# Kernel tuning notes

Measured on AMD Instinct MI355X. Metric: run time of the kernel, lower is better.

## Reference

```python
import jax, jax.numpy as jnp
import numpy as np

B, T, C, H = 4, 2048, 1024, 16
D = C // H  # head_dim = 64


def setup_inputs() -> dict:
    key = jax.random.key(0)
    k1, k2, k3 = jax.random.split(key, 3)
    x = jax.random.normal(k1, (B, T, C), dtype=jnp.float32)
    w_attn = jax.random.normal(k2, (C, 3 * C), dtype=jnp.float32) * (1.0 / np.sqrt(C))
    b_attn = jnp.zeros((3 * C,), dtype=jnp.float32)
    w_proj = jax.random.normal(k3, (C, C), dtype=jnp.float32) * (1.0 / np.sqrt(C))
    b_proj = jnp.zeros((C,), dtype=jnp.float32)
    return {"x": x, "w_attn": w_attn, "b_attn": b_attn, "w_proj": w_proj, "b_proj": b_proj}


def reference(x, w_attn, b_attn, w_proj, b_proj):
    Bx, Tx, Cx = x.shape
    qkv = x @ w_attn + b_attn                      # (B, T, 3C)
    q, k, v = jnp.split(qkv, 3, axis=2)
    # (B, T, C) -> (B, H, T, D)
    q = q.reshape(Bx, Tx, H, D).transpose(0, 2, 1, 3)
    k = k.reshape(Bx, Tx, H, D).transpose(0, 2, 1, 3)
    v = v.reshape(Bx, Tx, H, D).transpose(0, 2, 1, 3)
    scores = jnp.einsum('bhqd,bhkd->bhqk', q, k) / jnp.sqrt(jnp.float32(D))
    causal = jnp.tril(jnp.ones((Tx, Tx), dtype=bool))
    scores = jnp.where(causal[None, None], scores, jnp.float32(-jnp.inf))
    probs = jax.nn.softmax(scores, axis=-1)
    out = jnp.einsum('bhqk,bhkd->bhqd', probs, v)  # (B, H, T, D)
    out = out.transpose(0, 2, 1, 3).reshape(Bx, Tx, Cx)
    return out @ w_proj + b_proj
```

## Files before the change

### kernel.cpp

```cpp
#include <hip/hip_runtime.h>

#define AS1 __attribute__((address_space(1)))
#define AS3 __attribute__((address_space(3)))

using bf16x8  = __attribute__((ext_vector_type(8))) __bf16;
using floatx4 = __attribute__((ext_vector_type(4))) float;

#define SCQ 0.18033688f

__device__ inline ushort f2b(float f) {
    __bf16 h = (__bf16)f;
    return __builtin_bit_cast(ushort, h);
}

__global__ void k_prep(const float* __restrict__ x, ushort* __restrict__ xb,
                       const float* __restrict__ wa, ushort* __restrict__ waT,
                       const float* __restrict__ wp, ushort* __restrict__ wpT)
{
    __shared__ float tile[32][33];
    int blk = blockIdx.x;
    if (blk < 8192) {
        int i = (blk * 256 + threadIdx.x) * 4;
        float4 v = *(const float4*)(x + i);
        ushort4 o;
        o.x = f2b(v.x); o.y = f2b(v.y); o.z = f2b(v.z); o.w = f2b(v.w);
        *(ushort4*)(xb + i) = o;
        return;
    }
    const float* in; ushort* out; int R, Ncol, bx, by; float scale; int scale_cols;
    if (blk < 11264) {
        int idx = blk - 8192;
        in = wa; out = waT; R = 1024; Ncol = 3072;
        bx = idx % 96; by = idx / 96; scale = SCQ; scale_cols = 1024;
    } else {
        int idx = blk - 11264;
        in = wp; out = wpT; R = 1024; Ncol = 1024;
        bx = idx % 32; by = idx / 32; scale = 1.0f; scale_cols = 0;
    }
    int tx = threadIdx.x & 31, ty = threadIdx.x >> 5;
    int c0 = bx * 32, r0 = by * 32;
    for (int i = 0; i < 32; i += 8)
        tile[ty + i][tx] = in[(size_t)(r0 + ty + i) * Ncol + c0 + tx];
    __syncthreads();
    for (int i = 0; i < 32; i += 8) {
        int n = c0 + ty + i;
        float v = tile[tx][ty + i];
        if (n < scale_cols) v *= scale;
        out[(size_t)n * R + r0 + tx] = f2b(v);
    }
}

__global__ __launch_bounds__(256, 2) void k_gemm_bt(
    const ushort* __restrict__ A, const ushort* __restrict__ Bt,
    const float* __restrict__ bias, float* __restrict__ outv,
    int M, int N, int K)
{
    __shared__ __align__(16) ushort As[128 * 64];
    __shared__ __align__(16) ushort Bs[128 * 64];
    int tid = threadIdx.x;
    int m0 = blockIdx.y * 128, n0 = blockIdx.x * 128;
    int lane = tid & 63;
    int wm = (tid >> 7) * 64;
    int wn = ((tid >> 6) & 1) * 64;
    int lr = lane & 15, quad = lane >> 4;

    floatx4 acc[4][4] = {};
    const ushort* ags[4]; const ushort* bgs[4]; int sdst[4];
    #pragma unroll
    for (int it = 0; it < 4; ++it) {
        int slot = tid + 256 * it;
        int row = slot >> 3, ch = slot & 7;
        ags[it] = A  + (size_t)(m0 + row) * K + ch * 8;
        bgs[it] = Bt + (size_t)(n0 + row) * K + ch * 8;
        sdst[it] = slot * 8;
    }

    for (int kt = 0; kt < K; kt += 64) {
        #pragma unroll
        for (int it = 0; it < 4; ++it) {
            __builtin_amdgcn_global_load_lds((const AS1 unsigned int*)(ags[it] + kt),
                                             (AS3 unsigned int*)&As[sdst[it]], 16, 0, 0);
            __builtin_amdgcn_global_load_lds((const AS1 unsigned int*)(bgs[it] + kt),
                                             (AS3 unsigned int*)&Bs[sdst[it]], 16, 0, 0);
        }
        asm volatile("s_waitcnt vmcnt(0)" ::: "memory");
        __syncthreads();
        bf16x8 af[4][2], bf[4][2];
        #pragma unroll
        for (int i = 0; i < 4; ++i) {
            af[i][0] = *(const bf16x8*)&As[(wm + 16 * i + lr) * 64 + quad * 8];
            af[i][1] = *(const bf16x8*)&As[(wm + 16 * i + lr) * 64 + 32 + quad * 8];
        }
        #pragma unroll
        for (int j = 0; j < 4; ++j) {
            bf[j][0] = *(const bf16x8*)&Bs[(wn + 16 * j + lr) * 64 + quad * 8];
            bf[j][1] = *(const bf16x8*)&Bs[(wn + 16 * j + lr) * 64 + 32 + quad * 8];
        }
        #pragma unroll
        for (int i = 0; i < 4; ++i)
            #pragma unroll
            for (int j = 0; j < 4; ++j) {
                acc[i][j] = __builtin_amdgcn_mfma_f32_16x16x32_bf16(af[i][0], bf[j][0], acc[i][j], 0, 0, 0);
                acc[i][j] = __builtin_amdgcn_mfma_f32_16x16x32_bf16(af[i][1], bf[j][1], acc[i][j], 0, 0, 0);
            }
        __syncthreads();
    }

    #pragma unroll
    for (int j = 0; j < 4; ++j) {
        int col = n0 + wn + 16 * j + lr;
        float bv = bias[col];
        #pragma unroll
        for (int i = 0; i < 4; ++i) {
            int row = m0 + wm + 16 * i + quad * 4;
            #pragma unroll
            for (int r = 0; r < 4; ++r)
                outv[(size_t)(row + r) * N + col] = acc[i][j][r] + bv;
        }
    }
}

__global__ __launch_bounds__(256, 2) void k_gemm_qkv(
    const ushort* __restrict__ A, const ushort* __restrict__ Bt,
    const float* __restrict__ bias, ushort* __restrict__ qkv, ushort* __restrict__ vt)
{
    constexpr int K = 1024;
    __shared__ __align__(16) ushort As[128 * 64];
    __shared__ __align__(16) ushort Bs[128 * 64];
    int tid = threadIdx.x;
    int m0 = blockIdx.y * 128, n0 = blockIdx.x * 128;
    int lane = tid & 63;
    int wm = (tid >> 7) * 64;
    int wn = ((tid >> 6) & 1) * 64;
    int lr = lane & 15, quad = lane >> 4;

    floatx4 acc[4][4] = {};
    const ushort* ags[4]; const ushort* bgs[4]; int sdst[4];
    #pragma unroll
    for (int it = 0; it < 4; ++it) {
        int slot = tid + 256 * it;
        int row = slot >> 3, ch = slot & 7;
        ags[it] = A  + (size_t)(m0 + row) * K + ch * 8;
        bgs[it] = Bt + (size_t)(n0 + row) * K + ch * 8;
        sdst[it] = slot * 8;
    }

    for (int kt = 0; kt < K; kt += 64) {
        #pragma unroll
        for (int it = 0; it < 4; ++it) {
            __builtin_amdgcn_global_load_lds((const AS1 unsigned int*)(ags[it] + kt),
                                             (AS3 unsigned int*)&As[sdst[it]], 16, 0, 0);
            __builtin_amdgcn_global_load_lds((const AS1 unsigned int*)(bgs[it] + kt),
                                             (AS3 unsigned int*)&Bs[sdst[it]], 16, 0, 0);
        }
        asm volatile("s_waitcnt vmcnt(0)" ::: "memory");
        __syncthreads();
        bf16x8 af[4][2], bf[4][2];
        #pragma unroll
        for (int i = 0; i < 4; ++i) {
            af[i][0] = *(const bf16x8*)&As[(wm + 16 * i + lr) * 64 + quad * 8];
            af[i][1] = *(const bf16x8*)&As[(wm + 16 * i + lr) * 64 + 32 + quad * 8];
        }
        #pragma unroll
        for (int j = 0; j < 4; ++j) {
            bf[j][0] = *(const bf16x8*)&Bs[(wn + 16 * j + lr) * 64 + quad * 8];
            bf[j][1] = *(const bf16x8*)&Bs[(wn + 16 * j + lr) * 64 + 32 + quad * 8];
        }
        #pragma unroll
        for (int i = 0; i < 4; ++i)
            #pragma unroll
            for (int j = 0; j < 4; ++j) {
                acc[i][j] = __builtin_amdgcn_mfma_f32_16x16x32_bf16(af[i][0], bf[j][0], acc[i][j], 0, 0, 0);
                acc[i][j] = __builtin_amdgcn_mfma_f32_16x16x32_bf16(af[i][1], bf[j][1], acc[i][j], 0, 0, 0);
            }
        __syncthreads();
    }

    int bb = m0 >> 11;
    #pragma unroll
    for (int j = 0; j < 4; ++j) {
        int col = n0 + wn + 16 * j + lr;
        float bv = bias[col];
        if (col < 1024) bv *= SCQ;
        if (col < 2048) {
            #pragma unroll
            for (int i = 0; i < 4; ++i) {
                int row = m0 + wm + 16 * i + quad * 4;
                #pragma unroll
                for (int r = 0; r < 4; ++r)
                    qkv[(size_t)(row + r) * 2048 + col] = f2b(acc[i][j][r] + bv);
            }
        } else {
            int h = (col - 2048) >> 6, d = (col - 2048) & 63;
            ushort* vbase = vt + ((size_t)(bb * 16 + h) * 64 + d) * 2048;
            #pragma unroll
            for (int i = 0; i < 4; ++i) {
                int t0 = (m0 + wm + 16 * i + quad * 4) & 2047;
                ushort4 pk;
                ((ushort*)&pk)[0] = f2b(acc[i][j][0] + bv);
                ((ushort*)&pk)[1] = f2b(acc[i][j][1] + bv);
                ((ushort*)&pk)[2] = f2b(acc[i][j][2] + bv);
                ((ushort*)&pk)[3] = f2b(acc[i][j][3] + bv);
                *(ushort4*)&vbase[t0] = pk;
            }
        }
    }
}

__global__ __launch_bounds__(512, 4) void k_attn(const ushort* __restrict__ qkv,
                                                 const ushort* __restrict__ vt,
                                                 ushort* __restrict__ out)
{
    constexpr int T = 2048, SQK = 2048, C = 1024;
    __shared__ __align__(16) ushort Ks[64 * 64];
    __shared__ __align__(16) ushort Vs[64 * 64];
    __shared__ __align__(16) ushort Ps[8 * 16 * 72];
    int tid = threadIdx.x;
    int lane = tid & 63, wave = tid >> 6;
    int lr = lane & 15, quad = lane >> 4, lk = quad * 8;
    int bh = blockIdx.y;
    int b = bh >> 4, h = bh & 15;
    size_t base = (size_t)b * T * SQK;
    const ushort* kg0 = qkv + base + 1024 + h * 64;
    const ushort* vg0 = vt + (size_t)bh * 64 * 2048;
    ushort* psw = &Ps[wave * 16 * 72];

    int srow = tid >> 3;
    int sg   = (tid & 7) ^ (srow & 7);
    ushort* ksdst = &Ks[tid * 8];
    ushort* vsdst = &Vs[tid * 8];
    const ushort* kgs = kg0 + (size_t)srow * SQK + sg * 8;
    const ushort* vgs = vg0 + (size_t)srow * 2048 + sg * 8;

    bf16x8 ones;
    #pragma unroll
    for (int i = 0; i < 8; ++i) ones[i] = (__bf16)1.0f;
    int c0 = (quad ^ (lr & 7)) * 8;
    int c1 = ((4 + quad) ^ (lr & 7)) * 8;

    int qts[2] = { (int)blockIdx.x, 15 - (int)blockIdx.x };
    for (int ti = 0; ti < 2; ++ti) {
        int qt = qts[ti];
        int qrow = qt * 128 + wave * 16;
        int kt_d = qrow >> 6;
        const ushort* qp = qkv + base + (size_t)(qrow + lr) * SQK + h * 64;
        bf16x8 aq0 = *(const bf16x8*)(qp + lk);
        bf16x8 aq1 = *(const bf16x8*)(qp + 32 + lk);
        floatx4 o[4] = {};
        floatx4 lacc = {};
        int ktmax = 2 * qt + 1;

        for (int kt = 0; kt <= ktmax; ++kt) {
            __syncthreads();
            __builtin_amdgcn_global_load_lds((const AS1 unsigned int*)(kgs + (size_t)kt * 64 * SQK),
                                             (AS3 unsigned int*)ksdst, 16, 0, 0);
            __builtin_amdgcn_global_load_lds((const AS1 unsigned int*)(vgs + kt * 64),
                                             (AS3 unsigned int*)vsdst, 16, 0, 0);
            asm volatile("s_waitcnt vmcnt(0)" ::: "memory");
            __syncthreads();
            if (kt > kt_d) continue;

            floatx4 s[4];
            #pragma unroll
            for (int j = 0; j < 4; ++j) {
                const ushort* kr = &Ks[(16 * j + lr) * 64];
                bf16x8 bk0 = *(const bf16x8*)(kr + c0);
                bf16x8 bk1 = *(const bf16x8*)(kr + c1);
                floatx4 z = {};
                s[j] = __builtin_amdgcn_mfma_f32_16x16x32_bf16(aq0, bk0, z, 0, 0, 0);
                s[j] = __builtin_amdgcn_mfma_f32_16x16x32_bf16(aq1, bk1, s[j], 0, 0, 0);
            }
            if (kt == kt_d) {
                int qg = qrow + quad * 4, kb = kt * 64;
                #pragma unroll
                for (int r = 0; r < 4; ++r)
                    #pragma unroll
                    for (int j = 0; j < 4; ++j) {
                        float p = ((kb + 16 * j + lr) > (qg + r)) ? 0.f : exp2f(s[j][r]);
                        psw[(quad * 4 + r) * 72 + 16 * j + lr] = f2b(p);
                    }
            } else {
                #pragma unroll
                for (int r = 0; r < 4; ++r)
                    #pragma unroll
                    for (int j = 0; j < 4; ++j)
                        psw[(quad * 4 + r) * 72 + 16 * j + lr] = f2b(exp2f(s[j][r]));
            }
            asm volatile("s_waitcnt lgkmcnt(0)" ::: "memory");
            bf16x8 ap0 = *(const bf16x8*)&psw[lr * 72 + lk];
            bf16x8 ap1 = *(const bf16x8*)&psw[lr * 72 + 32 + lk];
            lacc = __builtin_amdgcn_mfma_f32_16x16x32_bf16(ap0, ones, lacc, 0, 0, 0);
            lacc = __builtin_amdgcn_mfma_f32_16x16x32_bf16(ap1, ones, lacc, 0, 0, 0);
            #pragma unroll
            for (int jd = 0; jd < 4; ++jd) {
                const ushort* vr = &Vs[(16 * jd + lr) * 64];
                bf16x8 bv0 = *(const bf16x8*)(vr + c0);
                bf16x8 bv1 = *(const bf16x8*)(vr + c1);
                o[jd] = __builtin_amdgcn_mfma_f32_16x16x32_bf16(ap0, bv0, o[jd], 0, 0, 0);
                o[jd] = __builtin_amdgcn_mfma_f32_16x16x32_bf16(ap1, bv1, o[jd], 0, 0, 0);
            }
        }

        #pragma unroll
        for (int r = 0; r < 4; ++r) {
            float inv = 1.0f / lacc[r];
            int row = b * T + qrow + quad * 4 + r;
            #pragma unroll
            for (int jd = 0; jd < 4; ++jd)
                out[(size_t)row * C + h * 64 + 16 * jd + lr] = f2b(o[jd][r] * inv);
        }
    }
}

extern "C" void kernel_launch(void* const* d_in, const int* in_sizes, int n_in,
                              void* d_out, int out_size, void* d_ws, size_t ws_size,
                              hipStream_t stream) {
    const float* x      = (const float*)d_in[0];
    const float* w_attn = (const float*)d_in[1];
    const float* b_attn = (const float*)d_in[2];
    const float* w_proj = (const float*)d_in[3];
    const float* b_proj = (const float*)d_in[4];
    float* out = (float*)d_out;

    constexpr int Bb = 4, T = 2048, C = 1024;
    constexpr int M = Bb * T;

    ushort* xb  = (ushort*)d_ws;
    ushort* waT = xb  + (size_t)M * C;
    ushort* wpT = waT + (size_t)3 * C * C;
    ushort* qkv = wpT + (size_t)C * C;
    ushort* vt  = qkv + (size_t)M * 2 * C;
    ushort* ao  = vt  + (size_t)64 * 64 * T;

    k_prep<<<12288, 256, 0, stream>>>(x, xb, w_attn, waT, w_proj, wpT);
    k_gemm_qkv<<<dim3(3 * C / 128, M / 128), 256, 0, stream>>>(xb, waT, b_attn, qkv, vt);
    k_attn<<<dim3(8, Bb * 16), 512, 0, stream>>>(qkv, vt, ao);
    k_gemm_bt<<<dim3(C / 128, M / 128), 256, 0, stream>>>(ao, wpT, b_proj, out, M, C, C);
}
```

Measured before the change: 258.1 us.

## Double-buffer K/V tiles and keep P in registers via permlane swaps

The attention kernel now double-buffers the K and V LDS tiles, issuing the global-to-LDS loads for the next key tile before computing on the current one, so the copy overlaps the MFMA work. It also computes S transposed (K as the A operand) and repacks the exponentiated scores into bf16 MFMA operands in registers with v_cvt_pk_bf16_f32 and permlane32/16 swaps. This removes the per-wave P staging buffer in LDS along with its store/wait/reload round trip. The trade-off is doubled K/V LDS usage, which may lower occupancy, and reliance on gfx950-specific permlane instructions.

```diff
diff --git a/kernel.cpp b/kernel.cpp
--- a/kernel.cpp
+++ b/kernel.cpp
@@ -11,6 +11,30 @@
 __device__ inline ushort f2b(float f) {
     __bf16 h = (__bf16)f;
     return __builtin_bit_cast(ushort, h);
+}
+
+__device__ inline unsigned cvtpk_bf16(float lo, float hi) {
+    unsigned r;
+    asm("v_cvt_pk_bf16_f32 %0, %1, %2" : "=v"(r) : "v"(lo), "v"(hi));
+    return r;
+}
+__device__ inline void plswap32(unsigned& a, unsigned& b) {
+    asm("v_permlane32_swap_b32 %0, %1" : "+v"(a), "+v"(b));
+}
+__device__ inline void plswap16(unsigned& a, unsigned& b) {
+    asm("v_permlane16_swap_b32 %0, %1" : "+v"(a), "+v"(b));
+}
+
+__device__ inline bf16x8 pack_swap(floatx4 ej0, floatx4 ej1) {
+    unsigned x0 = cvtpk_bf16(ej0[0], ej0[1]);
+    unsigned x1 = cvtpk_bf16(ej0[2], ej0[3]);
+    unsigned y0 = cvtpk_bf16(ej1[0], ej1[1]);
+    unsigned y1 = cvtpk_bf16(ej1[2], ej1[3]);
+    plswap32(x0, y0); plswap16(x0, y0);
+    plswap32(x1, y1); plswap16(x1, y1);
+    union { unsigned u[4]; bf16x8 v; } ua;
+    ua.u[0] = x0; ua.u[1] = x1; ua.u[2] = y0; ua.u[3] = y1;
+    return ua.v;
 }
 
 __global__ void k_prep(const float* __restrict__ x, ushort* __restrict__ xb,
@@ -212,9 +236,8 @@
                                                  ushort* __restrict__ out)
 {
     constexpr int T = 2048, SQK = 2048, C = 1024;
-    __shared__ __align__(16) ushort Ks[64 * 64];
-    __shared__ __align__(16) ushort Vs[64 * 64];
-    __shared__ __align__(16) ushort Ps[8 * 16 * 72];
+    __shared__ __align__(16) ushort Ks[2][64 * 64];
+    __shared__ __align__(16) ushort Vs[2][64 * 64];
     int tid = threadIdx.x;
     int lane = tid & 63, wave = tid >> 6;
     int lr = lane & 15, quad = lane >> 4, lk = quad * 8;
@@ -223,12 +246,10 @@
     size_t base = (size_t)b * T * SQK;
     const ushort* kg0 = qkv + base + 1024 + h * 64;
     const ushort* vg0 = vt + (size_t)bh * 64 * 2048;
-    ushort* psw = &Ps[wave * 16 * 72];
 
     int srow = tid >> 3;
     int sg   = (tid & 7) ^ (srow & 7);
-    ushort* ksdst = &Ks[tid * 8];
-    ushort* vsdst = &Vs[tid * 8];
+    int sdst = tid * 8;
     const ushort* kgs = kg0 + (size_t)srow * SQK + sg * 8;
     const ushort* vgs = vg0 + (size_t)srow * 2048 + sg * 8;
 
@@ -239,6 +260,7 @@
     int c1 = ((4 + quad) ^ (lr & 7)) * 8;
 
     int qts[2] = { (int)blockIdx.x, 15 - (int)blockIdx.x };
+    int cur = 0;
     for (int ti = 0; ti < 2; ++ti) {
         int qt = qts[ti];
         int qrow = qt * 128 + wave * 16;
@@ -250,55 +272,64 @@
         floatx4 lacc = {};
         int ktmax = 2 * qt + 1;
 
+        __builtin_amdgcn_global_load_lds((const AS1 unsigned int*)kgs,
+                                         (AS3 unsigned int*)&Ks[cur][sdst], 16, 0, 0);
+        __builtin_amdgcn_global_load_lds((const AS1 unsigned int*)vgs,
+                                         (AS3 unsigned int*)&Vs[cur][sdst], 16, 0, 0);
+        asm volatile("s_waitcnt vmcnt(0)" ::: "memory");
+        __syncthreads();
+
         for (int kt = 0; kt <= ktmax; ++kt) {
-            __syncthreads();
-            __builtin_amdgcn_global_load_lds((const AS1 unsigned int*)(kgs + (size_t)kt * 64 * SQK),
-                                             (AS3 unsigned int*)ksdst, 16, 0, 0);
-            __builtin_amdgcn_global_load_lds((const AS1 unsigned int*)(vgs + kt * 64),
-                                             (AS3 unsigned int*)vsdst, 16, 0, 0);
+            if (kt < ktmax) {
+                __builtin_amdgcn_global_load_lds((const AS1 unsigned int*)(kgs + (size_t)(kt + 1) * 64 * SQK),
+                                                 (AS3 unsigned int*)&Ks[cur ^ 1][sdst], 16, 0, 0);
+                __builtin_amdgcn_global_load_lds((const AS1 unsigned int*)(vgs + (kt + 1) * 64),
+                                                 (AS3 unsigned int*)&Vs[cur ^ 1][sdst], 16, 0, 0);
+            }
+            if (kt <= kt_d) {
+                const ushort* Kb = Ks[cur];
+                const ushort* Vb = Vs[cur];
+                floatx4 s[4];
+                #pragma unroll
+                for (int j = 0; j < 4; ++j) {
+                    const ushort* kr = &Kb[(16 * j + lr) * 64];
+                    bf16x8 bk0 = *(const bf16x8*)(kr + c0);
+                    bf16x8 bk1 = *(const bf16x8*)(kr + c1);
+                    floatx4 z = {};
+                    s[j] = __builtin_amdgcn_mfma_f32_16x16x32_bf16(bk0, aq0, z, 0, 0, 0);
+                    s[j] = __builtin_amdgcn_mfma_f32_16x16x32_bf16(bk1, aq1, s[j], 0, 0, 0);
+                }
+                floatx4 e[4];
+                if (kt == kt_d) {
+                    int qa = qrow + lr;
+                    #pragma unroll
+                    for (int j = 0; j < 4; ++j)
+                        #pragma unroll
+                        for (int r = 0; r < 4; ++r)
+                            e[j][r] = ((kt * 64 + 16 * j + quad * 4 + r) > qa) ? 0.f : exp2f(s[j][r]);
+                } else {
+                    #pragma unroll
+                    for (int j = 0; j < 4; ++j)
+                        #pragma unroll
+                        for (int r = 0; r < 4; ++r)
+                            e[j][r] = exp2f(s[j][r]);
+                }
+                bf16x8 ap0 = pack_swap(e[0], e[1]);
+                bf16x8 ap1 = pack_swap(e[2], e[3]);
+                lacc = __builtin_amdgcn_mfma_f32_16x16x32_bf16(ap0, ones, lacc, 0, 0, 0);
+                lacc = __builtin_amdgcn_mfma_f32_16x16x32_bf16(ap1, ones, lacc, 0, 0, 0);
+                #pragma unroll
+                for (int jd = 0; jd < 4; ++jd) {
+                    const ushort* vr = &Vb[(16 * jd + lr) * 64];
+                    bf16x8 bv0 = *(const bf16x8*)(vr + c0);
+                    bf16x8 bv1 = *(const bf16x8*)(vr + c1);
+                    o[jd] = __builtin_amdgcn_mfma_f32_16x16x32_bf16(ap0, bv0, o[jd], 0, 0, 0);
+                    o[jd] = __builtin_amdgcn_mfma_f32_16x16x32_bf16(ap1, bv1, o[jd], 0, 0, 0);
+                }
+            }
             asm volatile("s_waitcnt vmcnt(0)" ::: "memory");
             __syncthreads();
-            if (kt > kt_d) continue;
-
-            floatx4 s[4];
-            #pragma unroll
-            for (int j = 0; j < 4; ++j) {
-                const ushort* kr = &Ks[(16 * j + lr) * 64];
-                bf16x8 bk0 = *(const bf16x8*)(kr + c0);
-                bf16x8 bk1 = *(const bf16x8*)(kr + c1);
-                floatx4 z = {};
-                s[j] = __builtin_amdgcn_mfma_f32_16x16x32_bf16(aq0, bk0, z, 0, 0, 0);
-                s[j] = __builtin_amdgcn_mfma_f32_16x16x32_bf16(aq1, bk1, s[j], 0, 0, 0);
-            }
-            if (kt == kt_d) {
-                int qg = qrow + quad * 4, kb = kt * 64;
-                #pragma unroll
-                for (int r = 0; r < 4; ++r)
-                    #pragma unroll
-                    for (int j = 0; j < 4; ++j) {
-                        float p = ((kb + 16 * j + lr) > (qg + r)) ? 0.f : exp2f(s[j][r]);
-                        psw[(quad * 4 + r) * 72 + 16 * j + lr] = f2b(p);
-                    }
-            } else {
-                #pragma unroll
-                for (int r = 0; r < 4; ++r)
-                    #pragma unroll
-                    for (int j = 0; j < 4; ++j)
-                        psw[(quad * 4 + r) * 72 + 16 * j + lr] = f2b(exp2f(s[j][r]));
-            }
-            asm volatile("s_waitcnt lgkmcnt(0)" ::: "memory");
-            bf16x8 ap0 = *(const bf16x8*)&psw[lr * 72 + lk];
-            bf16x8 ap1 = *(const bf16x8*)&psw[lr * 72 + 32 + lk];
-            lacc = __builtin_amdgcn_mfma_f32_16x16x32_bf16(ap0, ones, lacc, 0, 0, 0);
-            lacc = __builtin_amdgcn_mfma_f32_16x16x32_bf16(ap1, ones, lacc, 0, 0, 0);
-            #pragma unroll
-            for (int jd = 0; jd < 4; ++jd) {
-                const ushort* vr = &Vs[(16 * jd + lr) * 64];
-                bf16x8 bv0 = *(const bf16x8*)(vr + c0);
-                bf16x8 bv1 = *(const bf16x8*)(vr + c1);
-                o[jd] = __builtin_amdgcn_mfma_f32_16x16x32_bf16(ap0, bv0, o[jd], 0, 0, 0);
-                o[jd] = __builtin_amdgcn_mfma_f32_16x16x32_bf16(ap1, bv1, o[jd], 0, 0, 0);
-            }
+            cur ^= 1;
         }
 
         #pragma unroll
```

New measurement: 256.2 us. No clear change (-0.7%).
